# Kernel optimization log

Hardware: AMD Instinct MI355X
Metric: run time of the kernel (lower is better)

## Reference

```python
import jax, jax.numpy as jnp
import numpy as np

N_NODES = 50000
N_EDGES = 800000
IN_CH = 64
OUT_CH = 128
POWERS = (0, 1, 2)


def setup_inputs() -> dict:
    key = jax.random.key(0)
    k1, k2, k3, k4 = jax.random.split(key, 4)
    x = jax.random.normal(k1, (N_NODES, IN_CH), dtype=jnp.float32)
    edge_index = jax.random.randint(k2, (2, N_EDGES), 0, N_NODES, dtype=jnp.int64)
    fan_in = IN_CH * len(POWERS)
    bound = 1.0 / np.sqrt(fan_in)
    W = jax.random.uniform(k3, (OUT_CH, fan_in), dtype=jnp.float32, minval=-bound, maxval=bound)
    b = jax.random.uniform(k4, (OUT_CH,), dtype=jnp.float32, minval=-bound, maxval=bound)
    return {"x": x, "edge_index": edge_index, "W": W, "b": b}


def _propagate_steps(x, edge_index, max_power):
    # propagated[0] = x; propagated[k] = scatter-add of propagated[k-1][src] into dst
    src, dst = edge_index[0], edge_index[1]
    hops = [x]
    h = x
    for _ in range(max_power):
        h = jax.ops.segment_sum(h[src], dst, num_segments=x.shape[0])
        hops.append(h)
    return hops


def reference(x, edge_index, W, b):
    hops = _propagate_steps(x, edge_index, max(POWERS))
    feats = jnp.concatenate([hops[p] for p in POWERS], axis=-1)  # [N, in*len(powers)]
    return feats @ W.T + b  # [N, out]
```

## Files before the change

kernel.cpp:

```cpp
#include <hip/hip_runtime.h>

#define N_NODES 50000
#define N_EDGES 800000
#define IN_CH   64
#define OUT_CH  128
#define FEAT    192
#define NB      ((N_NODES + 255) / 256)
#define EPB     1024
#define NPB     ((N_EDGES + EPB - 1) / EPB)
#define JPT     ((NPB + 255) / 256)
#define N_TILES (N_NODES / 16)

typedef __attribute__((ext_vector_type(8))) short short8;
typedef __attribute__((ext_vector_type(4))) float f32x4;

static __device__ __forceinline__ unsigned short f2bf(float f) {
  unsigned int u = __float_as_uint(f);
  u += 0x7FFFu + ((u >> 16) & 1u);
  return (unsigned short)(u >> 16);
}
static __device__ __forceinline__ float bf2f(unsigned int s) {
  return __uint_as_float(s << 16);
}

__global__ __launch_bounds__(256) void part_hist_kernel(
    const int* __restrict__ ei, int* __restrict__ hist) {
  __shared__ int lh[NB];
  const int b = blockIdx.x;
  for (int i = threadIdx.x; i < NB; i += 256) lh[i] = 0;
  __syncthreads();
  const int e0 = b * EPB;
  const int e1 = (e0 + EPB < N_EDGES) ? e0 + EPB : N_EDGES;
  for (int e = e0 + threadIdx.x; e < e1; e += 256)
    atomicAdd(&lh[((unsigned)ei[N_EDGES + e]) >> 8], 1);
  __syncthreads();
  for (int i = threadIdx.x; i < NB; i += 256) hist[b * NB + i] = lh[i];
}

__global__ __launch_bounds__(256) void part_scan_kernel(
    const int* __restrict__ hist, int* __restrict__ offs_t,
    int* __restrict__ total) {
  __shared__ int part[256];
  const int k = blockIdx.x;
  const int t = threadIdx.x;
  int loc[JPT];
  int sum = 0;
#pragma unroll
  for (int u = 0; u < JPT; ++u) {
    const int j = t * JPT + u;
    const int v = (j < NPB) ? hist[j * NB + k] : 0;
    loc[u] = v;
    sum += v;
  }
  part[t] = sum;
  __syncthreads();
  for (int off = 1; off < 256; off <<= 1) {
    const int v = (t >= off) ? part[t - off] : 0;
    __syncthreads();
    part[t] += v;
    __syncthreads();
  }
  int run = part[t] - sum;
#pragma unroll
  for (int u = 0; u < JPT; ++u) {
    const int j = t * JPT + u;
    if (j < NPB) offs_t[k * NPB + j] = run;
    run += loc[u];
  }
  if (t == 255) total[k] = part[255];
}

__global__ __launch_bounds__(256) void part_scan2_kernel(
    const int* __restrict__ total, int* __restrict__ boffset,
    int* __restrict__ rowptr) {
  __shared__ int s[256];
  const int tid = threadIdx.x;
  const int v = (tid < NB) ? total[tid] : 0;
  s[tid] = v;
  __syncthreads();
  for (int off = 1; off < 256; off <<= 1) {
    const int t = (tid >= off) ? s[tid - off] : 0;
    __syncthreads();
    s[tid] += t;
    __syncthreads();
  }
  if (tid < NB) boffset[tid] = s[tid] - v;
  if (tid == 0) {
    boffset[NB] = N_EDGES;
    rowptr[N_NODES] = N_EDGES;
  }
}

__global__ __launch_bounds__(256) void part_fill_kernel(
    const int* __restrict__ ei, const int* __restrict__ boffset,
    const int* __restrict__ offs_t, unsigned* __restrict__ pairs) {
  __shared__ int cur[NB];
  const int b = blockIdx.x;
  for (int k = threadIdx.x; k < NB; k += 256)
    cur[k] = boffset[k] + offs_t[k * NPB + b];
  __syncthreads();
  const int e0 = b * EPB;
  const int e1 = (e0 + EPB < N_EDGES) ? e0 + EPB : N_EDGES;
  for (int e = e0 + threadIdx.x; e < e1; e += 256) {
    const unsigned s = (unsigned)ei[e];
    const unsigned d = (unsigned)ei[N_EDGES + e];
    const int pos = atomicAdd(&cur[d >> 8], 1);
    pairs[pos] = (s << 8) | (d & 255u);
  }
}

__global__ __launch_bounds__(256) void bucket_csr_kernel(
    const unsigned* __restrict__ pairs, const int* __restrict__ boffset,
    int* __restrict__ rowptr, int* __restrict__ srcs) {
  __shared__ int cnt[256];
  __shared__ int sc[256];
  const int tid = threadIdx.x;
  const int base = boffset[blockIdx.x];
  const int limit = boffset[blockIdx.x + 1];

  cnt[tid] = 0;
  __syncthreads();
  for (int i = base + tid; i < limit; i += 256)
    atomicAdd(&cnt[pairs[i] & 255u], 1);
  __syncthreads();

  const int v = cnt[tid];
  sc[tid] = v;
  __syncthreads();
  for (int off = 1; off < 256; off <<= 1) {
    const int t = (tid >= off) ? sc[tid - off] : 0;
    __syncthreads();
    sc[tid] += t;
    __syncthreads();
  }
  const int ex = base + sc[tid] - v;

  const int node = blockIdx.x * 256 + tid;
  if (node < N_NODES) rowptr[node] = ex;

  cnt[tid] = ex;
  __syncthreads();
  for (int i = base + tid; i < limit; i += 256) {
    const unsigned p = pairs[i];
    const int pos = atomicAdd(&cnt[p & 255u], 1);
    srcs[pos] = (int)(p >> 8);
  }
}

__global__ __launch_bounds__(256) void cast_x_kernel(
    const float* __restrict__ x, unsigned short* __restrict__ xb) {
  const int t = blockIdx.x * blockDim.x + threadIdx.x;
  if (t >= (N_NODES * IN_CH) / 8) return;
  const float4 a = reinterpret_cast<const float4*>(x)[t * 2];
  const float4 c = reinterpret_cast<const float4*>(x)[t * 2 + 1];
  union { unsigned int u[4]; uint4 v; } o;
  o.u[0] = (unsigned)f2bf(a.x) | ((unsigned)f2bf(a.y) << 16);
  o.u[1] = (unsigned)f2bf(a.z) | ((unsigned)f2bf(a.w) << 16);
  o.u[2] = (unsigned)f2bf(c.x) | ((unsigned)f2bf(c.y) << 16);
  o.u[3] = (unsigned)f2bf(c.z) | ((unsigned)f2bf(c.w) << 16);
  reinterpret_cast<uint4*>(xb)[t] = o.v;
}

__global__ __launch_bounds__(256) void wfrag_kernel(
    const float* __restrict__ W, unsigned short* __restrict__ Wf) {
  const int t = blockIdx.x * blockDim.x + threadIdx.x;
  if (t >= 6 * 8 * 64 * 8) return;
  const int j = t & 7;
  const int l = (t >> 3) & 63;
  const int nt = (t >> 9) & 7;
  const int kk = t >> 12;
  const int o = nt * 16 + (l & 15);
  const int k = kk * 32 + (l >> 4) * 8 + j;
  Wf[t] = f2bf(W[o * FEAT + k]);
}

__global__ __launch_bounds__(256) void gather_kernel(
    const unsigned short* __restrict__ hin, const int* __restrict__ rowptr,
    const int* __restrict__ srcs, unsigned short* __restrict__ hout) {
  const int gid = blockIdx.x * blockDim.x + threadIdx.x;
  const int node = gid >> 6;
  if (node >= N_NODES) return;
  const int lane = threadIdx.x & 63;
  const int g = lane >> 3;
  const int s = lane & 7;

  const int beg = rowptr[node];
  const int end = rowptr[node + 1];

  float acc[8];
#pragma unroll
  for (int j = 0; j < 8; ++j) acc[j] = 0.0f;

  for (int i = beg + g; i < end; i += 8) {
    const int src = srcs[i];
    const uint4 v = *reinterpret_cast<const uint4*>(
        hin + (size_t)src * IN_CH + s * 8);
    acc[0] += bf2f(v.x & 0xffffu); acc[1] += bf2f(v.x >> 16);
    acc[2] += bf2f(v.y & 0xffffu); acc[3] += bf2f(v.y >> 16);
    acc[4] += bf2f(v.z & 0xffffu); acc[5] += bf2f(v.z >> 16);
    acc[6] += bf2f(v.w & 0xffffu); acc[7] += bf2f(v.w >> 16);
  }

#pragma unroll
  for (int j = 0; j < 8; ++j) {
    acc[j] += __shfl_xor(acc[j], 8);
    acc[j] += __shfl_xor(acc[j], 16);
    acc[j] += __shfl_xor(acc[j], 32);
  }

  if (g == 0) {
    union { unsigned int u[4]; uint4 v; } o;
    o.u[0] = (unsigned)f2bf(acc[0]) | ((unsigned)f2bf(acc[1]) << 16);
    o.u[1] = (unsigned)f2bf(acc[2]) | ((unsigned)f2bf(acc[3]) << 16);
    o.u[2] = (unsigned)f2bf(acc[4]) | ((unsigned)f2bf(acc[5]) << 16);
    o.u[3] = (unsigned)f2bf(acc[6]) | ((unsigned)f2bf(acc[7]) << 16);
    *reinterpret_cast<uint4*>(hout + (size_t)node * IN_CH + s * 8) = o.v;
  }
}

__global__ __launch_bounds__(256) void gemm_kernel(
    const unsigned short* __restrict__ xb,
    const unsigned short* __restrict__ h1b,
    const unsigned short* __restrict__ h2b,
    const unsigned short* __restrict__ Wf, const float* __restrict__ b,
    float* __restrict__ out) {
  const int wave = (blockIdx.x * 256 + threadIdx.x) >> 6;
  if (wave >= N_TILES) return;
  const int lane = threadIdx.x & 63;
  const int node0 = wave * 16;
  const int mrow = lane & 15;
  const int kg = lane >> 4;

  f32x4 acc[8];
#pragma unroll
  for (int nt = 0; nt < 8; ++nt) acc[nt] = (f32x4){0.f, 0.f, 0.f, 0.f};

  const unsigned short* const srcarr[3] = {xb, h1b, h2b};
#pragma unroll
  for (int kk = 0; kk < 6; ++kk) {
    const unsigned short* a = srcarr[kk >> 1];
    const short8 af = *reinterpret_cast<const short8*>(
        a + (size_t)(node0 + mrow) * IN_CH + (kk & 1) * 32 + kg * 8);
#pragma unroll
    for (int nt = 0; nt < 8; ++nt) {
      const short8 bf = *reinterpret_cast<const short8*>(
          Wf + ((size_t)(kk * 8 + nt) * 64 + lane) * 8);
      acc[nt] = __builtin_amdgcn_mfma_f32_16x16x32_bf16(af, bf, acc[nt], 0, 0, 0);
    }
  }

#pragma unroll
  for (int nt = 0; nt < 8; ++nt) {
    const int oc = nt * 16 + mrow;
    const float bias = b[oc];
#pragma unroll
    for (int r = 0; r < 4; ++r) {
      out[(size_t)(node0 + kg * 4 + r) * OUT_CH + oc] = acc[nt][r] + bias;
    }
  }
}

extern "C" void kernel_launch(void* const* d_in, const int* in_sizes, int n_in,
                              void* d_out, int out_size, void* d_ws,
                              size_t ws_size, hipStream_t stream) {
  const float* x = (const float*)d_in[0];
  const int* ei = (const int*)d_in[1];
  const float* W = (const float*)d_in[2];
  const float* b = (const float*)d_in[3];
  float* out = (float*)d_out;

  char* p = (char*)d_ws;
  unsigned short* xb = (unsigned short*)p;  p += (size_t)N_NODES * IN_CH * 2;
  unsigned short* h1b = (unsigned short*)p; p += (size_t)N_NODES * IN_CH * 2;
  unsigned short* h2b = (unsigned short*)p;
  unsigned* pairs = (unsigned*)h2b;         p += (size_t)N_NODES * IN_CH * 2;
  unsigned short* Wf = (unsigned short*)p;  p += (size_t)FEAT * OUT_CH * 2;
  int* total = (int*)p;   p += (size_t)NB * 4;
  int* boffset = (int*)p; p += (size_t)(NB + 1) * 4;
  int* rowptr = (int*)p;  p += (size_t)(N_NODES + 1) * 4;
  int* srcs = (int*)p;    p += (size_t)N_EDGES * 4;
  int* hist = (int*)p;    p += (size_t)NPB * NB * 4;
  int* offs_t = (int*)p;

  part_hist_kernel<<<NPB, 256, 0, stream>>>(ei, hist);
  part_scan_kernel<<<NB, 256, 0, stream>>>(hist, offs_t, total);
  part_scan2_kernel<<<1, 256, 0, stream>>>(total, boffset, rowptr);
  part_fill_kernel<<<NPB, 256, 0, stream>>>(ei, boffset, offs_t, pairs);
  bucket_csr_kernel<<<NB, 256, 0, stream>>>(pairs, boffset, rowptr, srcs);

  cast_x_kernel<<<(N_NODES * IN_CH / 8 + 255) / 256, 256, 0, stream>>>(x, xb);
  wfrag_kernel<<<(FEAT * OUT_CH + 255) / 256, 256, 0, stream>>>(W, Wf);

  const int gblocks = (N_NODES * 64 + 255) / 256;
  gather_kernel<<<gblocks, 256, 0, stream>>>(xb, rowptr, srcs, h1b);
  gather_kernel<<<gblocks, 256, 0, stream>>>(h1b, rowptr, srcs, h2b);

  const int gemmblocks = (N_TILES + 3) / 4;
  gemm_kernel<<<gemmblocks, 256, 0, stream>>>(xb, h1b, h2b, Wf, b, out);
}
```

Measured before the change: 164.4 us.

## Shrink CSR buckets to 64 nodes and fuse x cast with W fragment prep

Changes the destination bucket size in the partitioned CSR build from 256 to 64 nodes, so there are about four times as many buckets, more blocks in part_scan and bucket_csr, and less work per bucket. The top-level scan now runs in a single 1024-thread block, and pairs moves out of h2b into its own aligned workspace buffer. The x-to-bf16 cast and the W fragment conversion are merged into one launch to save a kernel launch. In exchange, the hist and offs_t arrays grow fourfold, and bucket_csr uses only 64 of its 256 threads for the scan.

```diff
diff --git a/kernel.cpp b/kernel.cpp
--- a/kernel.cpp
+++ b/kernel.cpp
@@ -5,11 +5,13 @@
 #define IN_CH   64
 #define OUT_CH  128
 #define FEAT    192
-#define NB      ((N_NODES + 255) / 256)
+#define NB      ((N_NODES + 63) / 64)
 #define EPB     1024
 #define NPB     ((N_EDGES + EPB - 1) / EPB)
 #define JPT     ((NPB + 255) / 256)
 #define N_TILES (N_NODES / 16)
+#define CAST_BLOCKS  ((N_NODES * IN_CH / 8 + 255) / 256)
+#define WFRAG_BLOCKS ((FEAT * OUT_CH + 255) / 256)
 
 typedef __attribute__((ext_vector_type(8))) short short8;
 typedef __attribute__((ext_vector_type(4))) float f32x4;
@@ -32,7 +34,7 @@
   const int e0 = b * EPB;
   const int e1 = (e0 + EPB < N_EDGES) ? e0 + EPB : N_EDGES;
   for (int e = e0 + threadIdx.x; e < e1; e += 256)
-    atomicAdd(&lh[((unsigned)ei[N_EDGES + e]) >> 8], 1);
+    atomicAdd(&lh[((unsigned)ei[N_EDGES + e]) >> 6], 1);
   __syncthreads();
   for (int i = threadIdx.x; i < NB; i += 256) hist[b * NB + i] = lh[i];
 }
@@ -70,15 +72,15 @@
   if (t == 255) total[k] = part[255];
 }
 
-__global__ __launch_bounds__(256) void part_scan2_kernel(
+__global__ __launch_bounds__(1024) void part_scan2_kernel(
     const int* __restrict__ total, int* __restrict__ boffset,
     int* __restrict__ rowptr) {
-  __shared__ int s[256];
+  __shared__ int s[1024];
   const int tid = threadIdx.x;
   const int v = (tid < NB) ? total[tid] : 0;
   s[tid] = v;
   __syncthreads();
-  for (int off = 1; off < 256; off <<= 1) {
+  for (int off = 1; off < 1024; off <<= 1) {
     const int t = (tid >= off) ? s[tid - off] : 0;
     __syncthreads();
     s[tid] += t;
@@ -104,74 +106,76 @@
   for (int e = e0 + threadIdx.x; e < e1; e += 256) {
     const unsigned s = (unsigned)ei[e];
     const unsigned d = (unsigned)ei[N_EDGES + e];
-    const int pos = atomicAdd(&cur[d >> 8], 1);
-    pairs[pos] = (s << 8) | (d & 255u);
+    const int pos = atomicAdd(&cur[d >> 6], 1);
+    pairs[pos] = (s << 6) | (d & 63u);
   }
 }
 
 __global__ __launch_bounds__(256) void bucket_csr_kernel(
     const unsigned* __restrict__ pairs, const int* __restrict__ boffset,
     int* __restrict__ rowptr, int* __restrict__ srcs) {
-  __shared__ int cnt[256];
-  __shared__ int sc[256];
+  __shared__ int cnt[64];
+  __shared__ int sc[64];
   const int tid = threadIdx.x;
   const int base = boffset[blockIdx.x];
   const int limit = boffset[blockIdx.x + 1];
 
-  cnt[tid] = 0;
+  if (tid < 64) cnt[tid] = 0;
   __syncthreads();
   for (int i = base + tid; i < limit; i += 256)
-    atomicAdd(&cnt[pairs[i] & 255u], 1);
-  __syncthreads();
-
-  const int v = cnt[tid];
-  sc[tid] = v;
-  __syncthreads();
-  for (int off = 1; off < 256; off <<= 1) {
-    const int t = (tid >= off) ? sc[tid - off] : 0;
-    __syncthreads();
-    sc[tid] += t;
-    __syncthreads();
-  }
-  const int ex = base + sc[tid] - v;
-
-  const int node = blockIdx.x * 256 + tid;
-  if (node < N_NODES) rowptr[node] = ex;
-
-  cnt[tid] = ex;
-  __syncthreads();
+    atomicAdd(&cnt[pairs[i] & 63u], 1);
+  __syncthreads();
+
+  if (tid < 64) sc[tid] = cnt[tid];
+  __syncthreads();
+  for (int off = 1; off < 64; off <<= 1) {
+    int v = 0;
+    if (tid < 64 && tid >= off) v = sc[tid - off];
+    __syncthreads();
+    if (tid < 64) sc[tid] += v;
+    __syncthreads();
+  }
+
+  if (tid < 64) {
+    const int ex = base + sc[tid] - cnt[tid];
+    const int node = blockIdx.x * 64 + tid;
+    if (node < N_NODES) rowptr[node] = ex;
+    cnt[tid] = ex;
+  }
+  __syncthreads();
+
   for (int i = base + tid; i < limit; i += 256) {
     const unsigned p = pairs[i];
-    const int pos = atomicAdd(&cnt[p & 255u], 1);
-    srcs[pos] = (int)(p >> 8);
-  }
-}
-
-__global__ __launch_bounds__(256) void cast_x_kernel(
-    const float* __restrict__ x, unsigned short* __restrict__ xb) {
-  const int t = blockIdx.x * blockDim.x + threadIdx.x;
-  if (t >= (N_NODES * IN_CH) / 8) return;
-  const float4 a = reinterpret_cast<const float4*>(x)[t * 2];
-  const float4 c = reinterpret_cast<const float4*>(x)[t * 2 + 1];
-  union { unsigned int u[4]; uint4 v; } o;
-  o.u[0] = (unsigned)f2bf(a.x) | ((unsigned)f2bf(a.y) << 16);
-  o.u[1] = (unsigned)f2bf(a.z) | ((unsigned)f2bf(a.w) << 16);
-  o.u[2] = (unsigned)f2bf(c.x) | ((unsigned)f2bf(c.y) << 16);
-  o.u[3] = (unsigned)f2bf(c.z) | ((unsigned)f2bf(c.w) << 16);
-  reinterpret_cast<uint4*>(xb)[t] = o.v;
-}
-
-__global__ __launch_bounds__(256) void wfrag_kernel(
-    const float* __restrict__ W, unsigned short* __restrict__ Wf) {
-  const int t = blockIdx.x * blockDim.x + threadIdx.x;
-  if (t >= 6 * 8 * 64 * 8) return;
-  const int j = t & 7;
-  const int l = (t >> 3) & 63;
-  const int nt = (t >> 9) & 7;
-  const int kk = t >> 12;
-  const int o = nt * 16 + (l & 15);
-  const int k = kk * 32 + (l >> 4) * 8 + j;
-  Wf[t] = f2bf(W[o * FEAT + k]);
+    const int pos = atomicAdd(&cnt[p & 63u], 1);
+    srcs[pos] = (int)(p >> 6);
+  }
+}
+
+__global__ __launch_bounds__(256) void prep_kernel(
+    const float* __restrict__ x, const float* __restrict__ W,
+    unsigned short* __restrict__ xb, unsigned short* __restrict__ Wf) {
+  if (blockIdx.x < CAST_BLOCKS) {
+    const int t = blockIdx.x * 256 + threadIdx.x;
+    if (t >= (N_NODES * IN_CH) / 8) return;
+    const float4 a = reinterpret_cast<const float4*>(x)[t * 2];
+    const float4 c = reinterpret_cast<const float4*>(x)[t * 2 + 1];
+    union { unsigned int u[4]; uint4 v; } o;
+    o.u[0] = (unsigned)f2bf(a.x) | ((unsigned)f2bf(a.y) << 16);
+    o.u[1] = (unsigned)f2bf(a.z) | ((unsigned)f2bf(a.w) << 16);
+    o.u[2] = (unsigned)f2bf(c.x) | ((unsigned)f2bf(c.y) << 16);
+    o.u[3] = (unsigned)f2bf(c.z) | ((unsigned)f2bf(c.w) << 16);
+    reinterpret_cast<uint4*>(xb)[t] = o.v;
+  } else {
+    const int t = (blockIdx.x - CAST_BLOCKS) * 256 + threadIdx.x;
+    if (t >= FEAT * OUT_CH) return;
+    const int j = t & 7;
+    const int l = (t >> 3) & 63;
+    const int nt = (t >> 9) & 7;
+    const int kk = t >> 12;
+    const int o = nt * 16 + (l & 15);
+    const int k = kk * 32 + (l >> 4) * 8 + j;
+    Wf[t] = f2bf(W[o * FEAT + k]);
+  }
 }
 
 __global__ __launch_bounds__(256) void gather_kernel(
@@ -209,7 +213,7 @@
   }
 
   if (g == 0) {
-    union { unsigned int u[4]; uint4 v; } o;
+    union { unsigned u[4]; uint4 v; } o;
     o.u[0] = (unsigned)f2bf(acc[0]) | ((unsigned)f2bf(acc[1]) << 16);
     o.u[1] = (unsigned)f2bf(acc[2]) | ((unsigned)f2bf(acc[3]) << 16);
     o.u[2] = (unsigned)f2bf(acc[4]) | ((unsigned)f2bf(acc[5]) << 16);
@@ -270,26 +274,30 @@
   float* out = (float*)d_out;
 
   char* p = (char*)d_ws;
-  unsigned short* xb = (unsigned short*)p;  p += (size_t)N_NODES * IN_CH * 2;
-  unsigned short* h1b = (unsigned short*)p; p += (size_t)N_NODES * IN_CH * 2;
-  unsigned short* h2b = (unsigned short*)p;
-  unsigned* pairs = (unsigned*)h2b;         p += (size_t)N_NODES * IN_CH * 2;
-  unsigned short* Wf = (unsigned short*)p;  p += (size_t)FEAT * OUT_CH * 2;
-  int* total = (int*)p;   p += (size_t)NB * 4;
-  int* boffset = (int*)p; p += (size_t)(NB + 1) * 4;
-  int* rowptr = (int*)p;  p += (size_t)(N_NODES + 1) * 4;
-  int* srcs = (int*)p;    p += (size_t)N_EDGES * 4;
-  int* hist = (int*)p;    p += (size_t)NPB * NB * 4;
-  int* offs_t = (int*)p;
+  auto take = [&](size_t bytes) {
+    char* r = p;
+    p += (bytes + 255) & ~(size_t)255;
+    return r;
+  };
+  unsigned short* xb  = (unsigned short*)take((size_t)N_NODES * IN_CH * 2);
+  unsigned short* h1b = (unsigned short*)take((size_t)N_NODES * IN_CH * 2);
+  unsigned short* h2b = (unsigned short*)take((size_t)N_NODES * IN_CH * 2);
+  unsigned short* Wf  = (unsigned short*)take((size_t)FEAT * OUT_CH * 2);
+  int* total   = (int*)take((size_t)NB * 4);
+  int* boffset = (int*)take((size_t)(NB + 1) * 4);
+  int* rowptr  = (int*)take((size_t)(N_NODES + 1) * 4);
+  unsigned* pairs = (unsigned*)take((size_t)N_EDGES * 4);
+  int* srcs   = (int*)take((size_t)N_EDGES * 4);
+  int* hist   = (int*)take((size_t)NPB * NB * 4);
+  int* offs_t = (int*)take((size_t)NB * NPB * 4);
 
   part_hist_kernel<<<NPB, 256, 0, stream>>>(ei, hist);
   part_scan_kernel<<<NB, 256, 0, stream>>>(hist, offs_t, total);
-  part_scan2_kernel<<<1, 256, 0, stream>>>(total, boffset, rowptr);
+  part_scan2_kernel<<<1, 1024, 0, stream>>>(total, boffset, rowptr);
   part_fill_kernel<<<NPB, 256, 0, stream>>>(ei, boffset, offs_t, pairs);
   bucket_csr_kernel<<<NB, 256, 0, stream>>>(pairs, boffset, rowptr, srcs);
 
-  cast_x_kernel<<<(N_NODES * IN_CH / 8 + 255) / 256, 256, 0, stream>>>(x, xb);
-  wfrag_kernel<<<(FEAT * OUT_CH + 255) / 256, 256, 0, stream>>>(W, Wf);
+  prep_kernel<<<CAST_BLOCKS + WFRAG_BLOCKS, 256, 0, stream>>>(x, W, xb, Wf);
 
   const int gblocks = (N_NODES * 64 + 255) / 256;
   gather_kernel<<<gblocks, 256, 0, stream>>>(xb, rowptr, srcs, h1b);
```

Measured after the change: 168.0 us. 2.2% more time.

## Fuse histogram with cast/weight prep and fold bucket-offset scan into consumers

Applied to the files above, without the earlier changes.

Merges the edge histogram, x-to-bf16 cast and W fragment packing into one launch, drops the standalone bucket-offset scan kernel by recomputing the tiny prefix scan of bucket totals inside the fill and CSR kernels, and raises edges per block so the per-bucket scan becomes a single-pass 256-wide scan. The histogram is stored transposed for coalesced scan reads. The aim is fewer kernel launches and less serialized small work, at the cost of redundant prefix scans in every block and fewer, heavier histogram/fill blocks with more shared-atomic contention.

```diff
diff --git a/kernel.cpp b/kernel.cpp
--- a/kernel.cpp
+++ b/kernel.cpp
@@ -5,11 +5,12 @@
 #define IN_CH   64
 #define OUT_CH  128
 #define FEAT    192
-#define NB      ((N_NODES + 255) / 256)
-#define EPB     1024
+#define NBK     ((N_NODES + 255) / 256)
+#define EPB     4096
 #define NPB     ((N_EDGES + EPB - 1) / EPB)
-#define JPT     ((NPB + 255) / 256)
 #define N_TILES (N_NODES / 16)
+#define CAST_BLOCKS  ((N_NODES * IN_CH / 8 + 255) / 256)
+#define WFRAG_BLOCKS ((FEAT * OUT_CH + 255) / 256)
 
 typedef __attribute__((ext_vector_type(8))) short short8;
 typedef __attribute__((ext_vector_type(4))) float f32x4;
@@ -23,100 +24,118 @@
   return __uint_as_float(s << 16);
 }
 
-__global__ __launch_bounds__(256) void part_hist_kernel(
-    const int* __restrict__ ei, int* __restrict__ hist) {
-  __shared__ int lh[NB];
+__global__ __launch_bounds__(256) void hist_prep_kernel(
+    const int* __restrict__ ei, const float* __restrict__ x,
+    const float* __restrict__ W, int* __restrict__ hist_t,
+    unsigned short* __restrict__ xb, unsigned short* __restrict__ Wf) {
+  if (blockIdx.x < NPB) {
+    __shared__ int lh[NBK];
+    const int b = blockIdx.x;
+    for (int i = threadIdx.x; i < NBK; i += 256) lh[i] = 0;
+    __syncthreads();
+    const int e0 = b * EPB;
+    const int e1 = (e0 + EPB < N_EDGES) ? e0 + EPB : N_EDGES;
+    for (int e = e0 + threadIdx.x; e < e1; e += 256)
+      atomicAdd(&lh[((unsigned)ei[N_EDGES + e]) >> 8], 1);
+    __syncthreads();
+    for (int k = threadIdx.x; k < NBK; k += 256) hist_t[k * NPB + b] = lh[k];
+  } else if (blockIdx.x < NPB + CAST_BLOCKS) {
+    const int t = (blockIdx.x - NPB) * 256 + threadIdx.x;
+    if (t >= (N_NODES * IN_CH) / 8) return;
+    const float4 a = reinterpret_cast<const float4*>(x)[t * 2];
+    const float4 c = reinterpret_cast<const float4*>(x)[t * 2 + 1];
+    union { unsigned int u[4]; uint4 v; } o;
+    o.u[0] = (unsigned)f2bf(a.x) | ((unsigned)f2bf(a.y) << 16);
+    o.u[1] = (unsigned)f2bf(a.z) | ((unsigned)f2bf(a.w) << 16);
+    o.u[2] = (unsigned)f2bf(c.x) | ((unsigned)f2bf(c.y) << 16);
+    o.u[3] = (unsigned)f2bf(c.z) | ((unsigned)f2bf(c.w) << 16);
+    reinterpret_cast<uint4*>(xb)[t] = o.v;
+  } else {
+    const int t = (blockIdx.x - NPB - CAST_BLOCKS) * 256 + threadIdx.x;
+    if (t >= FEAT * OUT_CH) return;
+    const int j = t & 7;
+    const int l = (t >> 3) & 63;
+    const int nt = (t >> 9) & 7;
+    const int kk = t >> 12;
+    const int o = nt * 16 + (l & 15);
+    const int k = kk * 32 + (l >> 4) * 8 + j;
+    Wf[t] = f2bf(W[o * FEAT + k]);
+  }
+}
+
+__global__ __launch_bounds__(256) void part_scan_kernel(
+    const int* __restrict__ hist_t, int* __restrict__ offs_t,
+    int* __restrict__ total) {
+  __shared__ int s[256];
+  const int k = blockIdx.x;
+  const int t = threadIdx.x;
+  const int v = (t < NPB) ? hist_t[k * NPB + t] : 0;
+  s[t] = v;
+  __syncthreads();
+  for (int off = 1; off < 256; off <<= 1) {
+    const int u = (t >= off) ? s[t - off] : 0;
+    __syncthreads();
+    s[t] += u;
+    __syncthreads();
+  }
+  if (t < NPB) offs_t[k * NPB + t] = s[t] - v;
+  if (t == 255) total[k] = s[255];
+}
+
+__global__ __launch_bounds__(256) void part_fill_kernel(
+    const int* __restrict__ ei, const int* __restrict__ total,
+    const int* __restrict__ offs_t, unsigned* __restrict__ pairs) {
+  __shared__ int s[256];
+  __shared__ int cur[NBK];
   const int b = blockIdx.x;
-  for (int i = threadIdx.x; i < NB; i += 256) lh[i] = 0;
-  __syncthreads();
+  const int t = threadIdx.x;
+  const int v = (t < NBK) ? total[t] : 0;
+  s[t] = v;
+  __syncthreads();
+  for (int off = 1; off < 256; off <<= 1) {
+    const int u = (t >= off) ? s[t - off] : 0;
+    __syncthreads();
+    s[t] += u;
+    __syncthreads();
+  }
+  if (t < NBK) cur[t] = (s[t] - v) + offs_t[t * NPB + b];
+  __syncthreads();
+
   const int e0 = b * EPB;
   const int e1 = (e0 + EPB < N_EDGES) ? e0 + EPB : N_EDGES;
-  for (int e = e0 + threadIdx.x; e < e1; e += 256)
-    atomicAdd(&lh[((unsigned)ei[N_EDGES + e]) >> 8], 1);
-  __syncthreads();
-  for (int i = threadIdx.x; i < NB; i += 256) hist[b * NB + i] = lh[i];
-}
-
-__global__ __launch_bounds__(256) void part_scan_kernel(
-    const int* __restrict__ hist, int* __restrict__ offs_t,
-    int* __restrict__ total) {
-  __shared__ int part[256];
-  const int k = blockIdx.x;
-  const int t = threadIdx.x;
-  int loc[JPT];
-  int sum = 0;
-#pragma unroll
-  for (int u = 0; u < JPT; ++u) {
-    const int j = t * JPT + u;
-    const int v = (j < NPB) ? hist[j * NB + k] : 0;
-    loc[u] = v;
-    sum += v;
-  }
-  part[t] = sum;
-  __syncthreads();
-  for (int off = 1; off < 256; off <<= 1) {
-    const int v = (t >= off) ? part[t - off] : 0;
-    __syncthreads();
-    part[t] += v;
-    __syncthreads();
-  }
-  int run = part[t] - sum;
-#pragma unroll
-  for (int u = 0; u < JPT; ++u) {
-    const int j = t * JPT + u;
-    if (j < NPB) offs_t[k * NPB + j] = run;
-    run += loc[u];
-  }
-  if (t == 255) total[k] = part[255];
-}
-
-__global__ __launch_bounds__(256) void part_scan2_kernel(
-    const int* __restrict__ total, int* __restrict__ boffset,
-    int* __restrict__ rowptr) {
-  __shared__ int s[256];
-  const int tid = threadIdx.x;
-  const int v = (tid < NB) ? total[tid] : 0;
-  s[tid] = v;
-  __syncthreads();
-  for (int off = 1; off < 256; off <<= 1) {
-    const int t = (tid >= off) ? s[tid - off] : 0;
-    __syncthreads();
-    s[tid] += t;
-    __syncthreads();
-  }
-  if (tid < NB) boffset[tid] = s[tid] - v;
-  if (tid == 0) {
-    boffset[NB] = N_EDGES;
-    rowptr[N_NODES] = N_EDGES;
-  }
-}
-
-__global__ __launch_bounds__(256) void part_fill_kernel(
-    const int* __restrict__ ei, const int* __restrict__ boffset,
-    const int* __restrict__ offs_t, unsigned* __restrict__ pairs) {
-  __shared__ int cur[NB];
-  const int b = blockIdx.x;
-  for (int k = threadIdx.x; k < NB; k += 256)
-    cur[k] = boffset[k] + offs_t[k * NPB + b];
-  __syncthreads();
-  const int e0 = b * EPB;
-  const int e1 = (e0 + EPB < N_EDGES) ? e0 + EPB : N_EDGES;
-  for (int e = e0 + threadIdx.x; e < e1; e += 256) {
-    const unsigned s = (unsigned)ei[e];
+  for (int e = e0 + t; e < e1; e += 256) {
+    const unsigned sv = (unsigned)ei[e];
     const unsigned d = (unsigned)ei[N_EDGES + e];
     const int pos = atomicAdd(&cur[d >> 8], 1);
-    pairs[pos] = (s << 8) | (d & 255u);
+    pairs[pos] = (sv << 8) | (d & 255u);
   }
 }
 
 __global__ __launch_bounds__(256) void bucket_csr_kernel(
-    const unsigned* __restrict__ pairs, const int* __restrict__ boffset,
+    const unsigned* __restrict__ pairs, const int* __restrict__ total,
     int* __restrict__ rowptr, int* __restrict__ srcs) {
+  __shared__ int s[256];
+  __shared__ int bofs[NBK];
   __shared__ int cnt[256];
   __shared__ int sc[256];
   const int tid = threadIdx.x;
-  const int base = boffset[blockIdx.x];
-  const int limit = boffset[blockIdx.x + 1];
+  {
+    const int v = (tid < NBK) ? total[tid] : 0;
+    s[tid] = v;
+    __syncthreads();
+    for (int off = 1; off < 256; off <<= 1) {
+      const int u = (tid >= off) ? s[tid - off] : 0;
+      __syncthreads();
+      s[tid] += u;
+      __syncthreads();
+    }
+    if (tid < NBK) bofs[tid] = s[tid] - v;
+  }
+  __syncthreads();
+
+  const int k = blockIdx.x;
+  const int base = bofs[k];
+  const int limit = base + total[k];
 
   cnt[tid] = 0;
   __syncthreads();
@@ -128,15 +147,16 @@
   sc[tid] = v;
   __syncthreads();
   for (int off = 1; off < 256; off <<= 1) {
-    const int t = (tid >= off) ? sc[tid - off] : 0;
-    __syncthreads();
-    sc[tid] += t;
+    const int u = (tid >= off) ? sc[tid - off] : 0;
+    __syncthreads();
+    sc[tid] += u;
     __syncthreads();
   }
   const int ex = base + sc[tid] - v;
 
-  const int node = blockIdx.x * 256 + tid;
+  const int node = k * 256 + tid;
   if (node < N_NODES) rowptr[node] = ex;
+  if (k == 0 && tid == 0) rowptr[N_NODES] = N_EDGES;
 
   cnt[tid] = ex;
   __syncthreads();
@@ -145,33 +165,6 @@
     const int pos = atomicAdd(&cnt[p & 255u], 1);
     srcs[pos] = (int)(p >> 8);
   }
-}
-
-__global__ __launch_bounds__(256) void cast_x_kernel(
-    const float* __restrict__ x, unsigned short* __restrict__ xb) {
-  const int t = blockIdx.x * blockDim.x + threadIdx.x;
-  if (t >= (N_NODES * IN_CH) / 8) return;
-  const float4 a = reinterpret_cast<const float4*>(x)[t * 2];
-  const float4 c = reinterpret_cast<const float4*>(x)[t * 2 + 1];
-  union { unsigned int u[4]; uint4 v; } o;
-  o.u[0] = (unsigned)f2bf(a.x) | ((unsigned)f2bf(a.y) << 16);
-  o.u[1] = (unsigned)f2bf(a.z) | ((unsigned)f2bf(a.w) << 16);
-  o.u[2] = (unsigned)f2bf(c.x) | ((unsigned)f2bf(c.y) << 16);
-  o.u[3] = (unsigned)f2bf(c.z) | ((unsigned)f2bf(c.w) << 16);
-  reinterpret_cast<uint4*>(xb)[t] = o.v;
-}
-
-__global__ __launch_bounds__(256) void wfrag_kernel(
-    const float* __restrict__ W, unsigned short* __restrict__ Wf) {
-  const int t = blockIdx.x * blockDim.x + threadIdx.x;
-  if (t >= 6 * 8 * 64 * 8) return;
-  const int j = t & 7;
-  const int l = (t >> 3) & 63;
-  const int nt = (t >> 9) & 7;
-  const int kk = t >> 12;
-  const int o = nt * 16 + (l & 15);
-  const int k = kk * 32 + (l >> 4) * 8 + j;
-  Wf[t] = f2bf(W[o * FEAT + k]);
 }
 
 __global__ __launch_bounds__(256) void gather_kernel(
@@ -209,7 +202,7 @@
   }
 
   if (g == 0) {
-    union { unsigned int u[4]; uint4 v; } o;
+    union { unsigned u[4]; uint4 v; } o;
     o.u[0] = (unsigned)f2bf(acc[0]) | ((unsigned)f2bf(acc[1]) << 16);
     o.u[1] = (unsigned)f2bf(acc[2]) | ((unsigned)f2bf(acc[3]) << 16);
     o.u[2] = (unsigned)f2bf(acc[4]) | ((unsigned)f2bf(acc[5]) << 16);
@@ -270,26 +263,27 @@
   float* out = (float*)d_out;
 
   char* p = (char*)d_ws;
-  unsigned short* xb = (unsigned short*)p;  p += (size_t)N_NODES * IN_CH * 2;
-  unsigned short* h1b = (unsigned short*)p; p += (size_t)N_NODES * IN_CH * 2;
-  unsigned short* h2b = (unsigned short*)p;
-  unsigned* pairs = (unsigned*)h2b;         p += (size_t)N_NODES * IN_CH * 2;
-  unsigned short* Wf = (unsigned short*)p;  p += (size_t)FEAT * OUT_CH * 2;
-  int* total = (int*)p;   p += (size_t)NB * 4;
-  int* boffset = (int*)p; p += (size_t)(NB + 1) * 4;
-  int* rowptr = (int*)p;  p += (size_t)(N_NODES + 1) * 4;
-  int* srcs = (int*)p;    p += (size_t)N_EDGES * 4;
-  int* hist = (int*)p;    p += (size_t)NPB * NB * 4;
-  int* offs_t = (int*)p;
-
-  part_hist_kernel<<<NPB, 256, 0, stream>>>(ei, hist);
-  part_scan_kernel<<<NB, 256, 0, stream>>>(hist, offs_t, total);
-  part_scan2_kernel<<<1, 256, 0, stream>>>(total, boffset, rowptr);
-  part_fill_kernel<<<NPB, 256, 0, stream>>>(ei, boffset, offs_t, pairs);
-  bucket_csr_kernel<<<NB, 256, 0, stream>>>(pairs, boffset, rowptr, srcs);
-
-  cast_x_kernel<<<(N_NODES * IN_CH / 8 + 255) / 256, 256, 0, stream>>>(x, xb);
-  wfrag_kernel<<<(FEAT * OUT_CH + 255) / 256, 256, 0, stream>>>(W, Wf);
+  auto take = [&](size_t bytes) {
+    char* r = p;
+    p += (bytes + 255) & ~(size_t)255;
+    return r;
+  };
+  unsigned short* xb  = (unsigned short*)take((size_t)N_NODES * IN_CH * 2);
+  unsigned short* h1b = (unsigned short*)take((size_t)N_NODES * IN_CH * 2);
+  unsigned short* h2b = (unsigned short*)take((size_t)N_NODES * IN_CH * 2);
+  unsigned short* Wf  = (unsigned short*)take((size_t)FEAT * OUT_CH * 2);
+  int* total  = (int*)take((size_t)NBK * 4);
+  int* rowptr = (int*)take((size_t)(N_NODES + 1) * 4);
+  unsigned* pairs = (unsigned*)take((size_t)N_EDGES * 4);
+  int* srcs   = (int*)take((size_t)N_EDGES * 4);
+  int* hist_t = (int*)take((size_t)NBK * NPB * 4);
+  int* offs_t = (int*)take((size_t)NBK * NPB * 4);
+
+  hist_prep_kernel<<<NPB + CAST_BLOCKS + WFRAG_BLOCKS, 256, 0, stream>>>(
+      ei, x, W, hist_t, xb, Wf);
+  part_scan_kernel<<<NBK, 256, 0, stream>>>(hist_t, offs_t, total);
+  part_fill_kernel<<<NPB, 256, 0, stream>>>(ei, total, offs_t, pairs);
+  bucket_csr_kernel<<<NBK, 256, 0, stream>>>(pairs, total, rowptr, srcs);
 
   const int gblocks = (N_NODES * 64 + 255) / 256;
   gather_kernel<<<gblocks, 256, 0, stream>>>(xb, rowptr, srcs, h1b);
```

Result: no change. 163.5 us (-0.6%).
